# Performance work log

Measured on AMD Instinct MI355X. Metric: run time of the kernel, lower is better.

The kernel has to match this reference:

```python
import jax, jax.numpy as jnp
import numpy as np
import math

NUM_EXPERTS = 64
CAPACITY_FACTOR = 1.0


def reference(x, wg):
    # x: [S, D] tokens, wg: [E, D] router weight (torch Linear layout)
    S, D = x.shape
    E = wg.shape[0]
    capacity = int(CAPACITY_FACTOR * math.ceil(S / E))  # training-mode capacity

    logits = jnp.einsum('sd,ed->se', x, wg)              # [S, E]
    gates = jax.nn.softmax(logits, axis=1)               # [S, E]

    indices1_s = jnp.argmax(gates, axis=1)               # [S]
    mask1 = jax.nn.one_hot(indices1_s, E, dtype=gates.dtype)  # [S, E]

    gates1_s = jnp.sum(gates * mask1, axis=1)            # [S]
    locations1 = jnp.cumsum(mask1, axis=0) - 1.0         # fused_cumsum_sub_one, [S, E]

    # load-balancing auxiliary loss
    me = jnp.mean(gates, axis=0)                         # [E]
    ce = jnp.mean(mask1, axis=0)                         # [E]
    l_aux = jnp.mean(me * ce) * (E * E)

    # drop tokens over capacity
    mask1 = mask1 * (locations1 < capacity).astype(mask1.dtype)
    locations1_s = jnp.sum(locations1 * mask1, axis=1).astype(jnp.int32)  # [S]

    gates1 = gates1_s[:, None] * mask1                   # [S, E]
    locations1_sc = jax.nn.one_hot(locations1_s, capacity, dtype=gates1.dtype)  # [S, C]
    # bmm(gates1[:, :, 1], locations1_sc[:, 1, :]) -> outer product per token
    combine1_sec = gates1[:, :, None] * locations1_sc[:, None, :]  # [S, E, C]
    dispatch_mask = combine1_sec.astype(bool)
    return (l_aux, combine1_sec, dispatch_mask)


def setup_inputs() -> dict:
    key = jax.random.key(0)
    k1, k2 = jax.random.split(key)
    x = jax.random.normal(k1, (8192, 2048), dtype=jnp.float32)
    wg = jax.random.normal(k2, (NUM_EXPERTS, 2048), dtype=jnp.float32) * 0.02
    return {"x": x, "wg": wg}
```

## Files before the change

kernel.cpp:

```cpp
#include <hip/hip_runtime.h>
#include <cstdint>
#include <cstddef>

#define S_TOK 8192
#define DIM   2048
#define NE    64
#define CAP   128
#define KSPLIT 2
#define BS    32
#define DT    32

#define OFF_PART   0
#define OFF_IDX    1048576
#define OFF_GATE   1056768
#define OFF_LOC    1064960
#define OFF_MESUM  1073152
#define OFF_PROD   1073216

__global__ __launch_bounds__(256) void gemm_logits(
    const float* __restrict__ x, const float* __restrict__ wg,
    float* __restrict__ part)
{
    __shared__ float xs[BS][DT + 1];
    __shared__ float wsh[NE][DT + 1];

    const int sb  = blockIdx.x * BS;
    const int k   = blockIdx.y;
    const int d0  = k * (DIM / KSPLIT);
    const int tid = threadIdx.x;

    const int s_loc = (tid >> 4) * 2;
    const int e_loc = (tid & 15) * 4;

    float acc[2][4] = {{0.f,0.f,0.f,0.f},{0.f,0.f,0.f,0.f}};

    for (int t = 0; t < DIM / KSPLIT; t += DT) {
        {
            const int r = tid >> 3;
            const int c = (tid & 7) * 4;
            const float4 v = *reinterpret_cast<const float4*>(
                &x[(size_t)(sb + r) * DIM + d0 + t + c]);
            xs[r][c]   = v.x; xs[r][c+1] = v.y;
            xs[r][c+2] = v.z; xs[r][c+3] = v.w;
        }
        {
            const int r = tid >> 2;
            const int c = (tid & 3) * 8;
            const float4 v0 = *reinterpret_cast<const float4*>(
                &wg[(size_t)r * DIM + d0 + t + c]);
            const float4 v1 = *reinterpret_cast<const float4*>(
                &wg[(size_t)r * DIM + d0 + t + c + 4]);
            wsh[r][c]   = v0.x; wsh[r][c+1] = v0.y;
            wsh[r][c+2] = v0.z; wsh[r][c+3] = v0.w;
            wsh[r][c+4] = v1.x; wsh[r][c+5] = v1.y;
            wsh[r][c+6] = v1.z; wsh[r][c+7] = v1.w;
        }
        __syncthreads();
        #pragma unroll
        for (int d = 0; d < DT; ++d) {
            const float xv0 = xs[s_loc][d];
            const float xv1 = xs[s_loc + 1][d];
            const float w0 = wsh[e_loc][d];
            const float w1 = wsh[e_loc + 1][d];
            const float w2 = wsh[e_loc + 2][d];
            const float w3 = wsh[e_loc + 3][d];
            acc[0][0] += xv0 * w0; acc[0][1] += xv0 * w1;
            acc[0][2] += xv0 * w2; acc[0][3] += xv0 * w3;
            acc[1][0] += xv1 * w0; acc[1][1] += xv1 * w1;
            acc[1][2] += xv1 * w2; acc[1][3] += xv1 * w3;
        }
        __syncthreads();
    }
    #pragma unroll
    for (int i = 0; i < 2; ++i)
        #pragma unroll
        for (int j = 0; j < 4; ++j)
            part[((size_t)k * S_TOK + sb + s_loc + i) * NE + e_loc + j] = acc[i][j];
}

__global__ __launch_bounds__(256) void softmax_top1(
    const float* __restrict__ part, int* __restrict__ idx,
    float* __restrict__ gate, float* __restrict__ me_sum)
{
    const int lane = threadIdx.x & 63;
    const int wid  = threadIdx.x >> 6;
    const int gw   = blockIdx.x * 4 + wid;

    float me_acc = 0.f;
    for (int s = gw; s < S_TOK; s += 256) {
        const float l = part[(size_t)s * NE + lane]
                      + part[((size_t)S_TOK + s) * NE + lane];
        float m = l;
        #pragma unroll
        for (int o = 32; o; o >>= 1) m = fmaxf(m, __shfl_xor(m, o));
        const float ex = __expf(l - m);
        float sum = ex;
        #pragma unroll
        for (int o = 32; o; o >>= 1) sum += __shfl_xor(sum, o);
        float bv = l; int bi = lane;
        #pragma unroll
        for (int o = 32; o; o >>= 1) {
            const float ov = __shfl_xor(bv, o);
            const int   oi = __shfl_xor(bi, o);
            if (ov > bv || (ov == bv && oi < bi)) { bv = ov; bi = oi; }
        }
        const float g = ex / sum;
        me_acc += g;
        if (lane == bi) {
            idx[s]  = bi;
            gate[s] = g;
        }
    }
    atomicAdd(&me_sum[lane], me_acc);
}

__global__ __launch_bounds__(256) void scan_expert(
    const int* __restrict__ idx, const float* __restrict__ me_sum,
    int* __restrict__ loc, float* __restrict__ prod)
{
    const int e    = blockIdx.x;
    const int tid  = threadIdx.x;
    const int lane = tid & 63;
    const int wid  = tid >> 6;
    __shared__ int wsum[4];

    int running = 0;
    for (int c = 0; c < S_TOK; c += 256) {
        const int s = c + tid;
        const bool match = (idx[s] == e);
        const unsigned long long b = __ballot(match);
        const int before = __popcll(b & ((1ULL << lane) - 1ULL));
        if (lane == 0) wsum[wid] = __popcll(b);
        __syncthreads();
        int woff = 0;
        #pragma unroll
        for (int w = 0; w < 4; ++w) if (w < wid) woff += wsum[w];
        const int tot = wsum[0] + wsum[1] + wsum[2] + wsum[3];
        if (match) {
            const int pos = running + woff + before;
            loc[s] = (pos < CAP) ? pos : -1;
        }
        running += tot;
        __syncthreads();
    }
    if (tid == 0) {
        const float me = me_sum[e] / (float)S_TOK;
        const float ce = (float)running / (float)S_TOK;
        prod[e] = me * ce;
    }
}

__global__ __launch_bounds__(256) void scatter_out(
    const int* __restrict__ idx, const int* __restrict__ loc,
    const float* __restrict__ gate, const float* __restrict__ prod,
    float* __restrict__ out)
{
    if (blockIdx.x == 0 && threadIdx.x < 64) {
        float p = prod[threadIdx.x];
        #pragma unroll
        for (int o = 32; o; o >>= 1) p += __shfl_xor(p, o);
        if (threadIdx.x == 0) out[0] = p * (float)NE;
    }
    const int s = blockIdx.x * 256 + threadIdx.x;
    const int l = loc[s];
    if (l >= 0) {
        const size_t off = ((size_t)s * NE + idx[s]) * CAP + l;
        out[1 + off] = gate[s];
        out[1 + (size_t)S_TOK * NE * CAP + off] = 1.0f;
    }
}

extern "C" void kernel_launch(void* const* d_in, const int* in_sizes, int n_in,
                              void* d_out, int out_size, void* d_ws, size_t ws_size,
                              hipStream_t stream)
{
    const float* x  = (const float*)d_in[0];
    const float* wg = (const float*)d_in[1];
    float* out = (float*)d_out;
    float* ws  = (float*)d_ws;

    float* part   = ws + OFF_PART;
    int*   idx    = (int*)(ws + OFF_IDX);
    float* gate   = ws + OFF_GATE;
    int*   loc    = (int*)(ws + OFF_LOC);
    float* me_sum = ws + OFF_MESUM;
    float* prod   = ws + OFF_PROD;

    hipMemsetAsync(d_out, 0, (size_t)out_size * sizeof(float), stream);
    hipMemsetAsync(me_sum, 0, NE * sizeof(float), stream);

    dim3 ggrid(S_TOK / BS, KSPLIT);
    gemm_logits<<<ggrid, 256, 0, stream>>>(x, wg, part);
    softmax_top1<<<64, 256, 0, stream>>>(part, idx, gate, me_sum);
    scan_expert<<<NE, 256, 0, stream>>>(idx, me_sum, loc, prod);
    scatter_out<<<S_TOK / 256, 256, 0, stream>>>(idx, loc, gate, prod, out);
}
```

Before: 680.3 us.

## Fuse output zeroing into scatter kernel and replace atomic me-sum with partials

Removes the two hipMemsetAsync calls. Each block of a new per-token kernel now zeroes its own combine and dispatch slabs with vectorized stores, handling the misalignment caused by the one-float l_aux offset, and then writes the single nonzero entry. The atomic accumulation of expert gate means is replaced by per-warp partial rows that scan_expert reduces, which removes the need to pre-zero me_sum. The aim is to drop memset launches and fill the output in one pass. The cost is that 8192 blocks each store 32 KB per slab through a kernel fill rather than the driver memset.

```diff
diff --git a/kernel.cpp b/kernel.cpp
--- a/kernel.cpp
+++ b/kernel.cpp
@@ -14,8 +14,8 @@
 #define OFF_IDX    1048576
 #define OFF_GATE   1056768
 #define OFF_LOC    1064960
-#define OFF_MESUM  1073152
-#define OFF_PROD   1073216
+#define OFF_MEPART 1073152
+#define OFF_PROD   1089536
 
 __global__ __launch_bounds__(256) void gemm_logits(
     const float* __restrict__ x, const float* __restrict__ wg,
@@ -80,7 +80,7 @@
 
 __global__ __launch_bounds__(256) void softmax_top1(
     const float* __restrict__ part, int* __restrict__ idx,
-    float* __restrict__ gate, float* __restrict__ me_sum)
+    float* __restrict__ gate, float* __restrict__ me_part)
 {
     const int lane = threadIdx.x & 63;
     const int wid  = threadIdx.x >> 6;
@@ -111,18 +111,24 @@
             gate[s] = g;
         }
     }
-    atomicAdd(&me_sum[lane], me_acc);
+    me_part[(size_t)gw * NE + lane] = me_acc;
 }
 
 __global__ __launch_bounds__(256) void scan_expert(
-    const int* __restrict__ idx, const float* __restrict__ me_sum,
+    const int* __restrict__ idx, const float* __restrict__ me_part,
     int* __restrict__ loc, float* __restrict__ prod)
 {
     const int e    = blockIdx.x;
     const int tid  = threadIdx.x;
     const int lane = tid & 63;
     const int wid  = tid >> 6;
-    __shared__ int wsum[4];
+    __shared__ int   wsum[4];
+    __shared__ float redf[4];
+
+    float mp = me_part[(size_t)tid * NE + e];
+    #pragma unroll
+    for (int o = 32; o; o >>= 1) mp += __shfl_xor(mp, o);
+    if (lane == 0) redf[wid] = mp;
 
     int running = 0;
     for (int c = 0; c < S_TOK; c += 256) {
@@ -144,29 +150,46 @@
         __syncthreads();
     }
     if (tid == 0) {
-        const float me = me_sum[e] / (float)S_TOK;
+        const float me = (redf[0] + redf[1] + redf[2] + redf[3]) / (float)S_TOK;
         const float ce = (float)running / (float)S_TOK;
         prod[e] = me * ce;
     }
 }
 
-__global__ __launch_bounds__(256) void scatter_out(
+__global__ __launch_bounds__(256) void zero_scatter(
     const int* __restrict__ idx, const int* __restrict__ loc,
     const float* __restrict__ gate, const float* __restrict__ prod,
     float* __restrict__ out)
 {
-    if (blockIdx.x == 0 && threadIdx.x < 64) {
-        float p = prod[threadIdx.x];
+    const int s   = blockIdx.x;
+    const int tid = threadIdx.x;
+    float* cslab = out + 1 + (size_t)s * (NE * CAP);
+    float* dslab = cslab + (size_t)S_TOK * NE * CAP;
+
+    const float4 z = {0.f, 0.f, 0.f, 0.f};
+    if (tid < 3)        { cslab[tid]  = 0.f; dslab[tid]  = 0.f; }
+    else if (tid == 3)  { cslab[8191] = 0.f; dslab[8191] = 0.f; }
+    float4* cb = reinterpret_cast<float4*>(cslab + 3);
+    float4* db = reinterpret_cast<float4*>(dslab + 3);
+    #pragma unroll
+    for (int j = tid; j < 2047; j += 256) { cb[j] = z; db[j] = z; }
+
+    __syncthreads();
+
+    if (tid == 0) {
+        const int l = loc[s];
+        if (l >= 0) {
+            const int t = idx[s] * CAP + l;
+            cslab[t] = gate[s];
+            dslab[t] = 1.0f;
+        }
+    }
+    if (s == 0 && tid >= 64 && tid < 128) {
+        const int ln = tid - 64;
+        float p = prod[ln];
         #pragma unroll
         for (int o = 32; o; o >>= 1) p += __shfl_xor(p, o);
-        if (threadIdx.x == 0) out[0] = p * (float)NE;
-    }
-    const int s = blockIdx.x * 256 + threadIdx.x;
-    const int l = loc[s];
-    if (l >= 0) {
-        const size_t off = ((size_t)s * NE + idx[s]) * CAP + l;
-        out[1 + off] = gate[s];
-        out[1 + (size_t)S_TOK * NE * CAP + off] = 1.0f;
+        if (ln == 0) out[0] = p * (float)NE;
     }
 }
 
@@ -179,19 +202,16 @@
     float* out = (float*)d_out;
     float* ws  = (float*)d_ws;
 
-    float* part   = ws + OFF_PART;
-    int*   idx    = (int*)(ws + OFF_IDX);
-    float* gate   = ws + OFF_GATE;
-    int*   loc    = (int*)(ws + OFF_LOC);
-    float* me_sum = ws + OFF_MESUM;
-    float* prod   = ws + OFF_PROD;
-
-    hipMemsetAsync(d_out, 0, (size_t)out_size * sizeof(float), stream);
-    hipMemsetAsync(me_sum, 0, NE * sizeof(float), stream);
+    float* part    = ws + OFF_PART;
+    int*   idx     = (int*)(ws + OFF_IDX);
+    float* gate    = ws + OFF_GATE;
+    int*   loc     = (int*)(ws + OFF_LOC);
+    float* me_part = ws + OFF_MEPART;
+    float* prod    = ws + OFF_PROD;
 
     dim3 ggrid(S_TOK / BS, KSPLIT);
     gemm_logits<<<ggrid, 256, 0, stream>>>(x, wg, part);
-    softmax_top1<<<64, 256, 0, stream>>>(part, idx, gate, me_sum);
-    scan_expert<<<NE, 256, 0, stream>>>(idx, me_sum, loc, prod);
-    scatter_out<<<S_TOK / 256, 256, 0, stream>>>(idx, loc, gate, prod, out);
-}
+    softmax_top1<<<64, 256, 0, stream>>>(part, idx, gate, me_part);
+    scan_expert<<<NE, 256, 0, stream>>>(idx, me_part, loc, prod);
+    zero_scatter<<<S_TOK, 256, 0, stream>>>(idx, loc, gate, prod, out);
+}
```

Measured after the change: 693.6 us. About the same (+1.9%).
